# Performance work log

Hardware: AMD Instinct MI355X
Metric: run time of the kernel (lower is better)

Reference implementation:

```python
import jax, jax.numpy as jnp
import numpy as np

N_TF, N_GENES, W, FANIN, B = 1024, 20000, 4, 16, 128
M = N_GENES * W  # middle width = 80000


def _build_edges(rng):
    # layer 1: each of the M per-gene nodes draws FANIN random TF inputs
    out1 = np.repeat(np.arange(M, dtype=np.int32), FANIN)
    in1 = rng.integers(0, N_TF, size=M * FANIN).astype(np.int32)
    in1[-1] = N_TF - 1  # ensure full input dim is touched
    # layer 2: dense WxW block per gene (node i of gene g sees all W nodes of gene g)
    out2 = np.repeat(np.arange(M, dtype=np.int32), W)
    gene = np.arange(M, dtype=np.int32) // W
    in2 = (gene[:, None] * W + np.arange(W, dtype=np.int32)[None, :]).reshape(-1)
    # layer 3: each gene output sums its W nodes
    out3 = np.repeat(np.arange(N_GENES, dtype=np.int32), W)
    in3 = np.arange(M, dtype=np.int32)
    return out1, in1, out2, in2, out3, in3


def setup_inputs() -> dict:
    key = jax.random.key(0)
    ks = jax.random.split(key, 7)
    rng = np.random.default_rng(0)
    out1, in1, out2, in2, out3, in3 = _build_edges(rng)
    scale1 = 1.0 / np.sqrt(FANIN)
    scale2 = 1.0 / np.sqrt(W)
    return {
        "features": jax.random.normal(ks[0], (B, N_TF), jnp.float32),
        "w1": jax.random.normal(ks[1], (out1.shape[0],), jnp.float32) * scale1,
        "b1": jax.random.normal(ks[2], (M,), jnp.float32) * 0.01,
        "w2": jax.random.normal(ks[3], (out2.shape[0],), jnp.float32) * scale2,
        "b2": jax.random.normal(ks[4], (M,), jnp.float32) * 0.01,
        "w3": jax.random.normal(ks[5], (out3.shape[0],), jnp.float32) * scale2,
        "b3": jax.random.normal(ks[6], (N_GENES,), jnp.float32) * 0.01,
        "out1": jnp.asarray(out1), "in1": jnp.asarray(in1),
        "out2": jnp.asarray(out2), "in2": jnp.asarray(in2),
        "out3": jnp.asarray(out3), "in3": jnp.asarray(in3),
    }


def _sparse_linear(x, w, b, out_idx, in_idx):
    # x: [B, n_in]; per-edge gather-multiply-scatter, y[b, o] = sum_e w_e * x[b, in_e] + b_o
    contrib = x.T[in_idx] * w[:, None]                      # [nnz, B]
    y = jax.ops.segment_sum(contrib, out_idx, num_segments=b.shape[0])  # [n_out, B]
    return y.T + b


def reference(features, w1, b1, w2, b2, w3, b3, out1, in1, out2, in2, out3, in3):
    h = jnp.tanh(_sparse_linear(features, w1, b1, out1, in1))
    h = jnp.tanh(_sparse_linear(h, w2, b2, out2, in2))
    return _sparse_linear(h, w3, b3, out3, in3)  # [B, N_GENES]
```

## Files before the change

kernel.cpp:

```cpp
#include <hip/hip_runtime.h>
#include <hip/hip_fp16.h>

#define N_TF    1024
#define N_GENES 20000
#define WW      4
#define FANIN   16
#define BATCH   128
#define NNZ1    (N_GENES * WW * FANIN)

#define GENES_PER_BLOCK 8
#define NTHREADS        512
#define NBLK            (N_GENES / GENES_PER_BLOCK)
#define YROW            (BATCH + 2)

__device__ __forceinline__ float2 fast_tanh2(float a, float b) {
    const float ta = __expf(2.0f * a);
    const float tb = __expf(2.0f * b);
    const float da = ta + 1.0f;
    const float db = tb + 1.0f;
    const float r  = __builtin_amdgcn_rcpf(da * db);
    return make_float2(fmaf(-2.0f * db, r, 1.0f),
                       fmaf(-2.0f * da, r, 1.0f));
}

__global__ __launch_bounds__(256) void transpose_cvt_kernel(
    const float* __restrict__ in, __half* __restrict__ out)
{
    __shared__ float tile[32][33];
    const int bx = blockIdx.x;
    const int by = blockIdx.y;
    const int tx = threadIdx.x;
    const int ty = threadIdx.y;
#pragma unroll
    for (int k = 0; k < 32; k += 8)
        tile[ty + k][tx] = in[(by * 32 + ty + k) * N_TF + bx * 32 + tx];
    __syncthreads();
    const int b = by * 32 + tx;
#pragma unroll
    for (int k = 0; k < 32; k += 8) {
        const int tf = bx * 32 + ty + k;
        out[tf * BATCH + b] = __float2half(tile[tx][ty + k]);
    }
}

__global__ __launch_bounds__(NTHREADS, 8) void fused_kernel(
    const __half* __restrict__ xh,
    const float*  __restrict__ w1,
    const float*  __restrict__ b1,
    const int*    __restrict__ in1,
    const float*  __restrict__ w2,
    const float*  __restrict__ b2,
    const float*  __restrict__ w3,
    const float*  __restrict__ b3,
    float*        __restrict__ out)
{
    __shared__ float yt[GENES_PER_BLOCK * YROW];

    const int tid  = threadIdx.x;
    const int wid  = __builtin_amdgcn_readfirstlane(tid >> 6);
    const int lane = tid & 63;
    const int g    = blockIdx.x * GENES_PER_BLOCK + wid;

    const int eb = g * (WW * FANIN);
    __half2 acc[WW];
    const __half2 hz = __float2half2_rn(0.0f);
#pragma unroll
    for (int i = 0; i < WW; ++i) acc[i] = hz;

#pragma unroll
    for (int j = 0; j < FANIN; ++j) {
#pragma unroll
        for (int i = 0; i < WW; ++i) {
            const int e   = eb + i * FANIN + j;
            const int idx = __builtin_amdgcn_readfirstlane(in1[e]);
            const float wf = w1[e];
            const __half2 wv = __float2half2_rn(wf);
            const __half2 xv = *((const __half2*)(xh + idx * BATCH) + lane);
            acc[i] = __hfma2(wv, xv, acc[i]);
        }
    }

    float2 h1[WW];
#pragma unroll
    for (int i = 0; i < WW; ++i) {
        const float  bb = b1[g * WW + i];
        const float2 af = __half22float2(acc[i]);
        h1[i] = fast_tanh2(af.x + bb, af.y + bb);
    }

    float2 h2[WW];
#pragma unroll
    for (int i = 0; i < WW; ++i) {
        const float4 w  = *(const float4*)(w2 + g * 16 + i * 4);
        const float  bb = b2[g * WW + i];
        const float sx = bb + w.x * h1[0].x + w.y * h1[1].x
                            + w.z * h1[2].x + w.w * h1[3].x;
        const float sy = bb + w.x * h1[0].y + w.y * h1[1].y
                            + w.z * h1[2].y + w.w * h1[3].y;
        h2[i] = fast_tanh2(sx, sy);
    }

    const float4 wv = *(const float4*)(w3 + g * 4);
    const float  bv = b3[g];
    const float yx = bv + wv.x * h2[0].x + wv.y * h2[1].x
                        + wv.z * h2[2].x + wv.w * h2[3].x;
    const float yy = bv + wv.x * h2[0].y + wv.y * h2[1].y
                        + wv.z * h2[2].y + wv.w * h2[3].y;

    float2* ytw = (float2*)(yt + wid * YROW);
    ytw[lane] = make_float2(yx, yy);

    __syncthreads();

    const int g0 = blockIdx.x * GENES_PER_BLOCK;
#pragma unroll
    for (int it = 0; it < (BATCH * GENES_PER_BLOCK) / NTHREADS; ++it) {
        const int idx = it * NTHREADS + tid;
        const int gq  = idx & (GENES_PER_BLOCK - 1);
        const int b   = idx >> 3;
        out[b * N_GENES + g0 + gq] = yt[gq * YROW + b];
    }
}

extern "C" void kernel_launch(void* const* d_in, const int* in_sizes, int n_in,
                              void* d_out, int out_size, void* d_ws, size_t ws_size,
                              hipStream_t stream)
{
    const float* features = (const float*)d_in[0];
    const float* w1 = (const float*)d_in[1];
    const float* b1 = (const float*)d_in[2];
    const float* w2 = (const float*)d_in[3];
    const float* b2 = (const float*)d_in[4];
    const float* w3 = (const float*)d_in[5];
    const float* b3 = (const float*)d_in[6];
    const int*   in1 = (const int*)d_in[8];
    float* out = (float*)d_out;

    __half* xh = (__half*)d_ws;

    hipLaunchKernelGGL(transpose_cvt_kernel, dim3(32, 4), dim3(32, 8), 0, stream,
                       features, xh);
    hipLaunchKernelGGL(fused_kernel, dim3(NBLK), dim3(NTHREADS), 0, stream,
                       xh, w1, b1, in1, w2, b2, w3, b3, out);
}
```

Baseline: 116.4 us.

## Pre-pack edge indices and half weights, batch gathers, enlarge blocks

Adds a prep pass, merged into the transpose kernel, that packs each layer-1 edge into an 8-byte record: a byte offset plus a duplicated half2 weight, reordered so a wave reads them sequentially. The fused kernel issues 32 independent gathers before doing the FMAs, to expose memory-level parallelism. Block size grows to 1024 threads covering 16 genes. The cost is an extra pass that writes and then reads about 10 MB of packed records every call, plus much higher register pressure from the 32-element buffer.

Measured after the change: 120.4 us. 1.03x slower.

```diff
diff --git a/kernel.cpp b/kernel.cpp
--- a/kernel.cpp
+++ b/kernel.cpp
@@ -6,12 +6,15 @@
 #define WW      4
 #define FANIN   16
 #define BATCH   128
-#define NNZ1    (N_GENES * WW * FANIN)
+#define EPG     (WW * FANIN)
+#define NNZ1    (N_GENES * EPG)
 
-#define GENES_PER_BLOCK 8
-#define NTHREADS        512
-#define NBLK            (N_GENES / GENES_PER_BLOCK)
-#define YROW            (BATCH + 2)
+#define GPB      16
+#define NTHREADS 1024
+#define NBLK     (N_GENES / GPB)
+#define YROW     (BATCH + 2)
+
+typedef unsigned int uint32;
 
 __device__ __forceinline__ float2 fast_tanh2(float a, float b) {
     const float ta = __expf(2.0f * a);
@@ -23,60 +26,87 @@
                        fmaf(-2.0f * da, r, 1.0f));
 }
 
-__global__ __launch_bounds__(256) void transpose_cvt_kernel(
-    const float* __restrict__ in, __half* __restrict__ out)
+__global__ __launch_bounds__(256) void prep_kernel(
+    const float* __restrict__ features,
+    const int*   __restrict__ in1,
+    const float* __restrict__ w1,
+    __half*      __restrict__ xh,
+    uint2*       __restrict__ edges)
 {
-    __shared__ float tile[32][33];
-    const int bx = blockIdx.x;
-    const int by = blockIdx.y;
-    const int tx = threadIdx.x;
-    const int ty = threadIdx.y;
+    const int blk = blockIdx.x;
+    const int tid = threadIdx.x;
+    if (blk < 128) {
+        __shared__ float tile[32][33];
+        const int bx = blk & 31;
+        const int by = blk >> 5;
+        const int tx = tid & 31;
+        const int ty = tid >> 5;
 #pragma unroll
-    for (int k = 0; k < 32; k += 8)
-        tile[ty + k][tx] = in[(by * 32 + ty + k) * N_TF + bx * 32 + tx];
-    __syncthreads();
-    const int b = by * 32 + tx;
+        for (int k = 0; k < 32; k += 8)
+            tile[ty + k][tx] = features[(by * 32 + ty + k) * N_TF + bx * 32 + tx];
+        __syncthreads();
+        const int b = by * 32 + tx;
 #pragma unroll
-    for (int k = 0; k < 32; k += 8) {
-        const int tf = bx * 32 + ty + k;
-        out[tf * BATCH + b] = __float2half(tile[tx][ty + k]);
+        for (int k = 0; k < 32; k += 8) {
+            const int tf = bx * 32 + ty + k;
+            xh[tf * BATCH + b] = __float2half(tile[tx][ty + k]);
+        }
+    } else {
+        const int e = (blk - 128) * 256 + tid;
+        if (e < NNZ1) {
+            const int g  = e >> 6;
+            const int t  = e & 63;
+            const int i  = t & 3;
+            const int j  = t >> 2;
+            const int eo = (g << 6) + (i << 4) + j;
+            const uint32 idxb = ((uint32)in1[eo]) << 8;
+            const __half h   = __float2half(w1[eo]);
+            const uint32 u   = (uint32)__half_as_ushort(h);
+            edges[e] = make_uint2(idxb, (u << 16) | u);
+        }
     }
 }
 
-__global__ __launch_bounds__(NTHREADS, 8) void fused_kernel(
+__global__ __launch_bounds__(NTHREADS, 4) void fused_kernel(
     const __half* __restrict__ xh,
-    const float*  __restrict__ w1,
+    const uint2*  __restrict__ edges,
     const float*  __restrict__ b1,
-    const int*    __restrict__ in1,
     const float*  __restrict__ w2,
     const float*  __restrict__ b2,
     const float*  __restrict__ w3,
     const float*  __restrict__ b3,
     float*        __restrict__ out)
 {
-    __shared__ float yt[GENES_PER_BLOCK * YROW];
+    __shared__ float yt[GPB * YROW];
 
     const int tid  = threadIdx.x;
     const int wid  = __builtin_amdgcn_readfirstlane(tid >> 6);
     const int lane = tid & 63;
-    const int g    = blockIdx.x * GENES_PER_BLOCK + wid;
+    const int g    = blockIdx.x * GPB + wid;
+    const int voff = lane << 2;
 
-    const int eb = g * (WW * FANIN);
+    const uint2* __restrict__ rec = edges + (size_t)g * EPG;
     __half2 acc[WW];
     const __half2 hz = __float2half2_rn(0.0f);
 #pragma unroll
     for (int i = 0; i < WW; ++i) acc[i] = hz;
 
 #pragma unroll
-    for (int j = 0; j < FANIN; ++j) {
+    for (int half = 0; half < 2; ++half) {
+        const uint2* __restrict__ rh = rec + half * 32;
+        __half2 xv[32];
 #pragma unroll
-        for (int i = 0; i < WW; ++i) {
-            const int e   = eb + i * FANIN + j;
-            const int idx = __builtin_amdgcn_readfirstlane(in1[e]);
-            const float wf = w1[e];
-            const __half2 wv = __float2half2_rn(wf);
-            const __half2 xv = *((const __half2*)(xh + idx * BATCH) + lane);
-            acc[i] = __hfma2(wv, xv, acc[i]);
+        for (int t = 0; t < 32; ++t) {
+            const int rx = __builtin_amdgcn_readfirstlane((int)rh[t].x);
+            xv[t] = *(const __half2*)((const char*)xh + rx + voff);
+        }
+#pragma unroll
+        for (int t = 0; t < 32; ++t) {
+            const int ry = __builtin_amdgcn_readfirstlane((int)rh[t].y);
+            uint32 u = (uint32)ry;
+            __half2 wv;
+            __builtin_memcpy(&wv, &u, 4);
+            acc[t & 3] = __hfma2(wv, xv[t], acc[t & 3]);
         }
     }
 
@@ -100,24 +130,24 @@
         h2[i] = fast_tanh2(sx, sy);
     }
 
-    const float4 wv = *(const float4*)(w3 + g * 4);
-    const float  bv = b3[g];
-    const float yx = bv + wv.x * h2[0].x + wv.y * h2[1].x
-                        + wv.z * h2[2].x + wv.w * h2[3].x;
-    const float yy = bv + wv.x * h2[0].y + wv.y * h2[1].y
-                        + wv.z * h2[2].y + wv.w * h2[3].y;
+    const float4 wv3 = *(const float4*)(w3 + g * 4);
+    const float  bv  = b3[g];
+    const float yx = bv + wv3.x * h2[0].x + wv3.y * h2[1].x
+                        + wv3.z * h2[2].x + wv3.w * h2[3].x;
+    const float yy = bv + wv3.x * h2[0].y + wv3.y * h2[1].y
+                        + wv3.z * h2[2].y + wv3.w * h2[3].y;
 
     float2* ytw = (float2*)(yt + wid * YROW);
     ytw[lane] = make_float2(yx, yy);
 
     __syncthreads();
 
-    const int g0 = blockIdx.x * GENES_PER_BLOCK;
+    const int g0 = blockIdx.x * GPB;
 #pragma unroll
-    for (int it = 0; it < (BATCH * GENES_PER_BLOCK) / NTHREADS; ++it) {
+    for (int it = 0; it < (BATCH * GPB) / NTHREADS; ++it) {
         const int idx = it * NTHREADS + tid;
-        const int gq  = idx & (GENES_PER_BLOCK - 1);
-        const int b   = idx >> 3;
+        const int gq  = idx & (GPB - 1);
+        const int b   = idx >> 4;
         out[b * N_GENES + g0 + gq] = yt[gq * YROW + b];
     }
 }
@@ -136,10 +166,12 @@
     const int*   in1 = (const int*)d_in[8];
     float* out = (float*)d_out;
 
-    __half* xh = (__half*)d_ws;
+    __half* xh    = (__half*)d_ws;
+    uint2*  edges = (uint2*)((char*)d_ws + (size_t)N_TF * BATCH * sizeof(__half));
 
-    hipLaunchKernelGGL(transpose_cvt_kernel, dim3(32, 4), dim3(32, 8), 0, stream,
-                       features, xh);
+    const int pack_blocks = (NNZ1 + 255) / 256;
+    hipLaunchKernelGGL(prep_kernel, dim3(128 + pack_blocks), dim3(256), 0, stream,
+                       features, in1, w1, xh, edges);
     hipLaunchKernelGGL(fused_kernel, dim3(NBLK), dim3(NTHREADS), 0, stream,
-                       xh, w1, b1, in1, w2, b2, w3, b3, out);
+                       xh, edges, b1, w2, b2, w3, b3, out);
 }
```
